# Performance work log

Measured on AMD Instinct MI355X. Metric: run time of the kernel, lower is better.

Reference implementation:

```python
import jax
import jax.numpy as jnp
from jax import lax
import numpy as np

EPS = 1e-5
CLASS_COUNT = 1000

# conv specs: (out_c, in_c, k, pool_stride)
_SPECS = [(8, 1, 11, 1), (32, 8, 7, 2), (64, 32, 5, 2), (64, 64, 5, 2), (128, 64, 5, 2), (128, 128, 3, 2)]


def _maxpool3(x, stride):
    return lax.reduce_window(x, -jnp.inf, lax.max, (1, 1, 3, 3), (1, 1, stride, stride), 'VALID')


def _block(x, w, gamma, beta, pool_stride):
    # tanh soft-binarized weights (mode=1, w=1)
    wq = jnp.tanh(w)
    y = lax.conv_general_dilated(x, wq, (1, 1), 'VALID', dimension_numbers=('NCHW', 'OIHW', 'NCHW'))
    y = _maxpool3(y, pool_stride)
    # BatchNorm2d in training mode: batch statistics over (N,H,W), biased var
    mu = jnp.mean(y, axis=(0, 2, 3), keepdims=True)
    var = jnp.var(y, axis=(0, 2, 3), keepdims=True)
    y = (y - mu) * lax.rsqrt(var + EPS)
    y = y * gamma.reshape(1, -1, 1, 1) + beta.reshape(1, -1, 1, 1)
    # tanh soft-binarized activation (mode=1, w=1)
    return jnp.tanh(y)


def setup_inputs() -> dict:
    key = jax.random.key(0)
    keys = jax.random.split(key, 8)
    inp = {'x': jax.random.normal(keys[0], (128, 1, 227, 227), dtype=jnp.float32)}
    for i, (oc, ic, k, _) in enumerate(_SPECS):
        fan_in = ic * k * k
        inp[f'w{i+1}'] = jax.random.normal(keys[i + 1], (oc, ic, k, k), dtype=jnp.float32) / np.sqrt(fan_in)
        inp[f'g{i+1}'] = jnp.ones((oc,), dtype=jnp.float32)
        inp[f'b{i+1}'] = jnp.zeros((oc,), dtype=jnp.float32)
    inp['wl'] = jax.random.normal(keys[7], (CLASS_COUNT, 512), dtype=jnp.float32) / np.sqrt(512.0)
    return inp


def reference(x, w1, w2, w3, w4, w5, w6, g1, g2, g3, g4, g5, g6,
              b1, b2, b3, b4, b5, b6, wl):
    ws = (w1, w2, w3, w4, w5, w6)
    gs = (g1, g2, g3, g4, g5, g6)
    bs = (b1, b2, b3, b4, b5, b6)
    for i, (_, _, _, ps) in enumerate(_SPECS):
        x = _block(x, ws[i], gs[i], bs[i], ps)
    # flatten -> BinaryLinear (tanh-binarized weight, no bias)
    x = x.reshape(x.shape[0], -1)  # [B, 512]
    return x @ jnp.tanh(wl).T  # [B, classCount]
```

## Files before the change

### kernel.cpp

```cpp
#include <hip/hip_runtime.h>
#include <hip/hip_bf16.h>
#include <hip/hip_fp16.h>

using bf16 = __hip_bfloat16;
using f16  = _Float16;
using f16x8 = __attribute__((ext_vector_type(8))) _Float16;
using f32x4  = __attribute__((ext_vector_type(4))) float;
typedef unsigned long long u64;

__device__ __forceinline__ float b2f(bf16 v){ return __bfloat162float(v); }
__device__ __forceinline__ bf16 f2b(float v){ return __float2bfloat16(v); }
__device__ __forceinline__ float ldf(const float* p){ return *p; }
__device__ __forceinline__ float ldf(const bf16* p){ return b2f(*p); }
__device__ __forceinline__ float ldf(const __half* p){ return __half2float(*p); }
__device__ __forceinline__ void stf(float* p, float v){ *p = v; }
__device__ __forceinline__ void stf(bf16* p, float v){ *p = f2b(v); }
__device__ __forceinline__ void stf(__half* p, float v){ *p = __float2half(v); }

__device__ __forceinline__ float ftanh(float x){
    float t = __builtin_amdgcn_exp2f(x * 2.8853900817779268f);
    return 1.0f - 2.0f * __builtin_amdgcn_rcpf(t + 1.0f);
}

__device__ __forceinline__ float ld_any(const void* p, int i, int isBf16)
{
    return isBf16 ? b2f(((const bf16*)p)[i]) : ((const float*)p)[i];
}

__device__ __forceinline__ int det_bf(const void* g)
{
    return (*(const unsigned*)g == 0x3F803F80u) ? 1 : 0;
}

__device__ __forceinline__ void bn_pr(const float* __restrict__ sums,
                                      const void* __restrict__ g,
                                      const void* __restrict__ b,
                                      int bf, int C, float inv, int c,
                                      float& sc, float& sh)
{
    float mean = sums[c] * inv;
    float var  = sums[C + c] * inv - mean * mean;
    float rstd = rsqrtf(fmaxf(var, 0.f) + 1e-5f);
    sc = ld_any(g, c, bf) * rstd;
    sh = ld_any(b, c, bf) - mean * sc;
}

__global__ __launch_bounds__(256)
void prep_all(const void* __restrict__ w1, const void* __restrict__ w6,
              const void* __restrict__ wlw, const void* __restrict__ w2,
              const void* __restrict__ w3, const void* __restrict__ w4,
              const void* __restrict__ w5, const void* __restrict__ g1,
              float* __restrict__ wq0, float* __restrict__ wq5,
              float* __restrict__ wlqT, __half* __restrict__ wpk,
              __half* __restrict__ wpk3, __half* __restrict__ wpk4,
              __half* __restrict__ wpk5, int* __restrict__ flag)
{
    const int bf = det_bf(g1);
    const int b = blockIdx.x, t = threadIdx.x;
    if (b == 0 && t == 0) *flag = bf;
    if (b < 4) {
        int i = b * 256 + t;
        if (i < 968) wq0[i] = tanhf(ld_any(w1, i, bf));
    } else if (b < 580) {
        int i = (b - 4) * 256 + t;
        if (i < 147456) wq5[i] = tanhf(ld_any(w6, i, bf));
    } else if (b < 2580) {
        int i = (b - 580) * 256 + t;
        if (i < 512000) {
            int cls = i >> 9, k = i & 511;
            wlqT[k * 1000 + cls] = tanhf(ld_any(wlw, i, bf));
        }
    } else if (b < 2636) {
        int i = (b - 2580) * 256 + t;
        if (i < 14336) {
            int ic  = i & 7;
            int q   = (i >> 3) & 3;
            int col = (i >> 5) & 15;
            int g   = (i >> 9) & 1;
            int khg = (i >> 10) & 1;
            int kw  = i >> 11;
            int kh  = khg * 4 + q;
            int oc  = g * 16 + col;
            __half v = __float2half(0.f);
            if (kh < 7)
                v = __float2half(tanhf(ld_any(w2, (oc * 8 + ic) * 49 + kh * 7 + kw, bf)));
            wpk[i] = v;
        }
    } else if (b < 2836) {
        int i = (b - 2636) * 256 + t;
        if (i < 51200) {
            int tap = i >> 11;
            int g   = (i >> 9) & 3;
            int col = (i >> 5) & 15;
            int icp = i & 31;
            int oc  = g * 16 + col;
            wpk3[i] = __float2half(tanhf(ld_any(w3, (oc * 32 + icp) * 25 + tap, bf)));
        }
    } else if (b < 3236) {
        int i = (b - 2836) * 256 + t;
        if (i < 102400) {
            int step = i >> 11;
            int g    = (i >> 9) & 3;
            int col  = (i >> 5) & 15;
            int icp  = i & 31;
            int icg  = step / 25, tap = step - icg * 25;
            int oc   = g * 16 + col;
            int ic   = icg * 32 + icp;
            wpk4[i] = __float2half(tanhf(ld_any(w4, (oc * 64 + ic) * 25 + tap, bf)));
        }
    } else {
        int i = (b - 3236) * 256 + t;
        if (i < 204800) {
            int step = i >> 12;
            int ocg  = (i >> 11) & 1;
            int g    = (i >> 9) & 3;
            int col  = (i >> 5) & 15;
            int icp  = i & 31;
            int icg  = step / 25, tap = step - icg * 25;
            int oc   = ocg * 64 + g * 16 + col;
            int ic   = icg * 32 + icp;
            wpk5[i] = __float2half(tanhf(ld_any(w5, (oc * 64 + ic) * 25 + tap, bf)));
        }
    }
}

__global__ __launch_bounds__(256)
void b2conv(const __half* __restrict__ A1, const __half* __restrict__ wpk,
            __half* __restrict__ raw, float* __restrict__ sums2,
            const float* __restrict__ sums1, const void* __restrict__ g1,
            const void* __restrict__ b1)
{
    __shared__ __align__(16) char smem[32000];
    __shared__ float s_part[512];
    f16*   xs = (f16*)smem;
    float* pb = (float*)smem;

    const int tid = threadIdx.x;
    const int n   = blockIdx.z;
    const int ty  = blockIdx.x / 15, tx = blockIdx.x - ty * 15;
    const int cy0 = ty * 30, cx0 = tx * 14;

    const int bf1 = det_bf(g1);
    float ssc[8], ssh[8];
    #pragma unroll
    for (int j = 0; j < 8; j++)
        bn_pr(sums1, g1, b1, bf1, 8, 1.f / 5916800.f, j, ssc[j], ssh[j]);

    for (int i = tid; i < 858; i += 256) {
        int r = i / 22, c = i - r * 22;
        int gr = cy0 + r, gc = cx0 + c;
        f16x8 v = (f16x8){0, 0, 0, 0, 0, 0, 0, 0};
        if (gr < 215 && gc < 215)
            v = *(const f16x8*)((const f16*)A1 + ((size_t)(n * 215 + gr) * 215 + gc) * 8);
        f16x8 o;
        #pragma unroll
        for (int j = 0; j < 8; j++)
            o[j] = (f16)ftanh(fmaf((float)v[j], ssc[j], ssh[j]));
        *(f16x8*)(xs + i * 8) = o;
    }
    __syncthreads();

    const int lane = tid & 63, wid = tid >> 6;
    const int col = lane & 15, q = lane >> 4;
    const int arow = q * 22;

    f32x4 acc[8][2];
    #pragma unroll
    for (int f = 0; f < 8; f++)
        #pragma unroll
        for (int g = 0; g < 2; g++)
            acc[f][g] = (f32x4){0.f, 0.f, 0.f, 0.f};

    const f16* wb = (const f16*)wpk + col * 32 + q * 8;
    f16x8 wc0 = *(const f16x8*)(wb);
    f16x8 wc1 = *(const f16x8*)(wb + 512);

    #pragma unroll
    for (int s = 0; s < 14; s++) {
        f16x8 wn0 = wc0, wn1 = wc1;
        if (s < 13) {
            const f16* wn = wb + (s + 1) * 1024;
            wn0 = *(const f16x8*)(wn);
            wn1 = *(const f16x8*)(wn + 512);
        }
        int kw = s >> 1, khg = s & 1;
        int aoffs = arow + khg * 88 + kw;
        #pragma unroll
        for (int f = 0; f < 8; f++) {
            int gi = (wid * 8 + f) * 22 + col + aoffs;
            f16x8 a = *(const f16x8*)(xs + gi * 8);
            acc[f][0] = __builtin_amdgcn_mfma_f32_16x16x32_f16(a, wc0, acc[f][0], 0, 0, 0);
            acc[f][1] = __builtin_amdgcn_mfma_f32_16x16x32_f16(a, wc1, acc[f][1], 0, 0, 0);
        }
        wc0 = wn0; wc1 = wn1;
    }
    __syncthreads();

    for (int h = 0; h < 2; h++) {
        #pragma unroll
        for (int f = 0; f < 8; f++) {
            int cr = wid * 8 + f;
            if (cr < 31)
                *(f32x4*)(pb + col * 500 + cr * 16 + q * 4) = acc[f][h];
        }
        __syncthreads();
        const int ocl = tid >> 4, slot = tid & 15;
        float sm = 0.f, sq = 0.f;
        for (int j = slot; j < 105; j += 16) {
            int py = j / 7, px = j - (j / 7) * 7;
            int gph = ty * 15 + py, gpw = tx * 7 + px;
            if (gph < 104 && gpw < 104) {
                const float* cp = pb + ocl * 500 + (2 * py) * 16 + 2 * px;
                float m = cp[0];
                #pragma unroll
                for (int dy = 0; dy < 3; dy++)
                    #pragma unroll
                    for (int dx = 0; dx < 3; dx++)
                        m = fmaxf(m, cp[dy * 16 + dx]);
                int oc = h * 16 + ocl;
                size_t oidx = ((size_t)(n * 104 + gph) * 104 + gpw) * 32 + oc;
                raw[oidx] = __float2half(m);
                sm += m; sq += m * m;
            }
        }
        s_part[tid] = sm; s_part[256 + tid] = sq;
        __syncthreads();
        if (tid < 16) {
            float a = 0.f, b = 0.f;
            #pragma unroll
            for (int t = 0; t < 16; t++) {
                a += s_part[tid * 16 + t];
                b += s_part[256 + tid * 16 + t];
            }
            atomicAdd(&sums2[h * 16 + tid],      a);
            atomicAdd(&sums2[32 + h * 16 + tid], b);
        }
        __syncthreads();
    }
}

__global__ __launch_bounds__(256)
void b3conv(const __half* __restrict__ A2, const __half* __restrict__ wpk3,
            __half* __restrict__ A3t, float* __restrict__ sums3,
            const float* __restrict__ sums2, const void* __restrict__ g2,
            const void* __restrict__ b2)
{
    __shared__ __align__(16) char smem[32000];
    __shared__ float s_part[512];
    f16*   xs = (f16*)smem;
    float* pb = (float*)smem;

    const int tid = threadIdx.x;
    const int n   = blockIdx.z;
    const int ty  = blockIdx.x / 7, tx = blockIdx.x - ty * 7;
    const int y0  = ty * 14, x0 = tx * 14;

    if (tid < 32) {
        float sc, sh;
        bn_pr(sums2, g2, b2, det_bf(g2), 32, 1.f / 1384448.f, tid, sc, sh);
        s_part[tid] = sc; s_part[32 + tid] = sh;
    }
    __syncthreads();

    for (int i = tid; i < 1600; i += 256) {
        int pos = i >> 2, g8 = i & 3;
        int gy = y0 + pos / 20, gx = x0 + pos % 20;
        f16x8 v = *(const f16x8*)((const f16*)A2 +
                  ((size_t)(n * 104 + gy) * 104 + gx) * 32 + g8 * 8);
        int c0 = g8 * 8;
        f16x8 o;
        #pragma unroll
        for (int j = 0; j < 8; j++)
            o[j] = (f16)ftanh(fmaf((float)v[j], s_part[c0 + j], s_part[32 + c0 + j]));
        *(f16x8*)(xs + pos * 40 + g8 * 8) = o;
    }

    const int lane = tid & 63, wid = tid >> 6;
    const int col = lane & 15, q = lane >> 4;

    f32x4 acc[4][4];
    #pragma unroll
    for (int f = 0; f < 4; f++)
        #pragma unroll
        for (int g = 0; g < 4; g++)
            acc[f][g] = (f32x4){0.f, 0.f, 0.f, 0.f};

    const f16* wb = (const f16*)wpk3 + col * 32 + q * 8;
    f16x8 w[4];
    #pragma unroll
    for (int g = 0; g < 4; g++)
        w[g] = *(const f16x8*)(wb + g * 512);

    __syncthreads();

    #pragma unroll 1
    for (int tap = 0; tap < 25; tap++) {
        const f16* wnb = wb + (tap < 24 ? tap + 1 : tap) * 2048;
        f16x8 wn[4];
        #pragma unroll
        for (int g = 0; g < 4; g++)
            wn[g] = *(const f16x8*)(wnb + g * 512);

        int kh = tap / 5, kw = tap - (tap / 5) * 5;
        f16x8 a[4];
        #pragma unroll
        for (int f = 0; f < 4; f++) {
            int pos = (wid * 4 + f + kh) * 20 + col + kw;
            a[f] = *(const f16x8*)(xs + pos * 40 + q * 8);
        }
        #pragma unroll
        for (int g = 0; g < 4; g++)
            #pragma unroll
            for (int f = 0; f < 4; f++)
                acc[f][g] = __builtin_amdgcn_mfma_f32_16x16x32_f16(
                    a[f], w[g], acc[f][g], 0, 0, 0);
        #pragma unroll
        for (int g = 0; g < 4; g++)
            w[g] = wn[g];
    }

    for (int h = 0; h < 2; h++) {
        __syncthreads();
        #pragma unroll
        for (int f = 0; f < 4; f++) {
            int cr = wid * 4 + f;
            if (cr < 15) {
                #pragma unroll
                for (int gg = 0; gg < 2; gg++)
                    *(f32x4*)(pb + (gg * 16 + col) * 244 + cr * 16 + q * 4) = acc[f][h * 2 + gg];
            }
        }
        __syncthreads();
        const int ocl = tid >> 3, slot = tid & 7;
        float sm = 0.f, sq = 0.f;
        for (int j = slot; j < 49; j += 8) {
            int py = j / 7, px = j - (j / 7) * 7;
            const float* cp = pb + ocl * 244 + (2 * py) * 16 + 2 * px;
            float m = cp[0];
            #pragma unroll
            for (int dy = 0; dy < 3; dy++)
                #pragma unroll
                for (int dx = 0; dx < 3; dx++)
                    m = fmaxf(m, cp[dy * 16 + dx]);
            int gph = ty * 7 + py, gpw = tx * 7 + px;
            A3t[((size_t)(n * 49 + gph) * 49 + gpw) * 64 + h * 32 + ocl]
                = __float2half(m);
            sm += m; sq += m * m;
        }
        s_part[tid] = sm; s_part[256 + tid] = sq;
        __syncthreads();
        if (tid < 32) {
            float a = 0.f, b = 0.f;
            #pragma unroll
            for (int t = 0; t < 8; t++) {
                a += s_part[tid * 8 + t];
                b += s_part[256 + tid * 8 + t];
            }
            atomicAdd(&sums3[h * 32 + tid],      a);
            atomicAdd(&sums3[64 + h * 32 + tid], b);
        }
    }
}

__global__ __launch_bounds__(256)
void b4conv(const __half* __restrict__ A3t, const __half* __restrict__ wpk4,
            __half* __restrict__ A4, float* __restrict__ sums4,
            const float* __restrict__ sums3, const void* __restrict__ g3,
            const void* __restrict__ b3)
{
    __shared__ __align__(16) char smem[31232];
    __shared__ float s_part[512];
    __shared__ float s_ss[128];
    f16*   xs = (f16*)smem;
    float* pb = (float*)smem;

    const int tid = threadIdx.x;
    const int n   = blockIdx.z;
    const int ty  = blockIdx.x >> 2, tx = blockIdx.x & 3;
    const int y0  = ty * 14, x0 = tx * 14;
    const int lane = tid & 63, wid = tid >> 6;
    const int col = lane & 15, q = lane >> 4;

    if (tid < 64) {
        float sc, sh;
        bn_pr(sums3, g3, b3, det_bf(g3), 64, 1.f / 307328.f, tid, sc, sh);
        s_ss[tid] = sc; s_ss[64 + tid] = sh;
    }

    f32x4 acc[4][4];
    #pragma unroll
    for (int f = 0; f < 4; f++)
        #pragma unroll
        for (int g = 0; g < 4; g++)
            acc[f][g] = (f32x4){0.f, 0.f, 0.f, 0.f};

    const f16* wb = (const f16*)wpk4 + col * 32 + q * 8;
    f16x8 w[4];
    #pragma unroll
    for (int g = 0; g < 4; g++)
        w[g] = *(const f16x8*)(wb + g * 512);

    #pragma unroll 1
    for (int icg = 0; icg < 2; icg++) {
        __syncthreads();
        for (int i = tid; i < 1520; i += 256) {
            int pos = i >> 2, g8 = i & 3;
            int gy = y0 + pos / 20, gx = x0 + pos % 20;
            f16x8 o = (f16x8){0, 0, 0, 0, 0, 0, 0, 0};
            if (gy < 49 && gx < 49) {
                f16x8 v = *(const f16x8*)((const f16*)A3t +
                    ((size_t)(n * 49 + gy) * 49 + gx) * 64 + icg * 32 + g8 * 8);
                int c0 = icg * 32 + g8 * 8;
                #pragma unroll
                for (int j = 0; j < 8; j++)
                    o[j] = (f16)ftanh(fmaf((float)v[j], s_ss[c0 + j], s_ss[64 + c0 + j]));
            }
            *(f16x8*)(xs + pos * 40 + g8 * 8) = o;
        }
        __syncthreads();

        #pragma unroll 1
        for (int tap = 0; tap < 25; tap++) {
            int step = icg * 25 + tap;
            const f16* wnb = wb + (size_t)(step < 49 ? step + 1 : step) * 2048;
            f16x8 wn[4];
            #pragma unroll
            for (int g = 0; g < 4; g++)
                wn[g] = *(const f16x8*)(wnb + g * 512);

            int kh = tap / 5, kw = tap - (tap / 5) * 5;
            f16x8 a[4];
            #pragma unroll
            for (int f = 0; f < 4; f++) {
                int r = wid * 4 + f + kh; if (r > 18) r = 18;
                int pos = r * 20 + col + kw;
                a[f] = *(const f16x8*)(xs + pos * 40 + q * 8);
            }
            #pragma unroll
            for (int g = 0; g < 4; g++)
                #pragma unroll
                for (int f = 0; f < 4; f++)
                    acc[f][g] = __builtin_amdgcn_mfma_f32_16x16x32_f16(
                        a[f], w[g], acc[f][g], 0, 0, 0);
            #pragma unroll
            for (int g = 0; g < 4; g++)
                w[g] = wn[g];
        }
    }

    for (int h = 0; h < 2; h++) {
        __syncthreads();
        #pragma unroll
        for (int f = 0; f < 4; f++) {
            int cr = wid * 4 + f;
            if (cr < 15) {
                #pragma unroll
                for (int gg = 0; gg < 2; gg++)
                    *(f32x4*)(pb + (gg * 16 + col) * 244 + cr * 16 + q * 4) = acc[f][h * 2 + gg];
            }
        }
        __syncthreads();
        const int ocl = tid >> 3, slot = tid & 7;
        float sm = 0.f, sq = 0.f;
        for (int j = slot; j < 49; j += 8) {
            int py = j / 7, px = j - (j / 7) * 7;
            int gph = ty * 7 + py, gpw = tx * 7 + px;
            if (gph < 22 && gpw < 22) {
                const float* cp = pb + ocl * 244 + (2 * py) * 16 + 2 * px;
                float m = cp[0];
                #pragma unroll
                for (int dy = 0; dy < 3; dy++)
                    #pragma unroll
                    for (int dx = 0; dx < 3; dx++)
                        m = fmaxf(m, cp[dy * 16 + dx]);
                A4[((size_t)(n * 22 + gph) * 22 + gpw) * 64 + h * 32 + ocl]
                    = __float2half(m);
                sm += m; sq += m * m;
            }
        }
        s_part[tid] = sm; s_part[256 + tid] = sq;
        __syncthreads();
        if (tid < 32) {
            float a = 0.f, b = 0.f;
            #pragma unroll
            for (int t = 0; t < 8; t++) {
                a += s_part[tid * 8 + t];
                b += s_part[256 + tid * 8 + t];
            }
            atomicAdd(&sums4[h * 32 + tid],      a);
            atomicAdd(&sums4[64 + h * 32 + tid], b);
        }
    }
}

__global__ __launch_bounds__(256)
void b5conv(const __half* __restrict__ A4, const __half* __restrict__ wpk5,
            float* __restrict__ A5, float* __restrict__ sums5,
            const float* __restrict__ sums4, const void* __restrict__ g4,
            const void* __restrict__ b4)
{
    __shared__ __align__(16) char smem[49664];
    __shared__ float s_part[512];
    __shared__ float s_ss[128];
    f16*   xs = (f16*)smem;
    float* pb = (float*)smem;

    const int tid = threadIdx.x;
    const int n   = blockIdx.z;
    const int ocg = blockIdx.x;
    const int lane = tid & 63, wid = tid >> 6;
    const int col = lane & 15, q = lane >> 4;

    if (tid < 64) {
        float sc, sh;
        bn_pr(sums4, g4, b4, det_bf(g4), 64, 1.f / 61952.f, tid, sc, sh);
        s_ss[tid] = sc; s_ss[64 + tid] = sh;
    }

    int abase[6];
    #pragma unroll
    for (int f = 0; f < 6; f++) {
        int m = (wid * 6 + f) * 16 + col;
        if (m > 323) m = 323;
        int r = m / 18, cc = m - r * 18;
        abase[f] = r * 22 + cc;
    }

    f32x4 acc[6][4];
    #pragma unroll
    for (int f = 0; f < 6; f++)
        #pragma unroll
        for (int g = 0; g < 4; g++)
            acc[f][g] = (f32x4){0.f, 0.f, 0.f, 0.f};

    const f16* wb = (const f16*)wpk5 + ocg * 2048 + col * 32 + q * 8;
    f16x8 w[4];
    #pragma unroll
    for (int g = 0; g < 4; g++)
        w[g] = *(const f16x8*)(wb + g * 512);

    #pragma unroll 1
    for (int icg = 0; icg < 2; icg++) {
        __syncthreads();
        for (int i = tid; i < 1936; i += 256) {
            int pos = i >> 2, g8 = i & 3;
            f16x8 v = *(const f16x8*)((const f16*)A4 + ((size_t)(n * 484 + pos)) * 64
                                      + icg * 32 + g8 * 8);
            int c0 = icg * 32 + g8 * 8;
            f16x8 o;
            #pragma unroll
            for (int j = 0; j < 8; j++)
                o[j] = (f16)ftanh(fmaf((float)v[j], s_ss[c0 + j], s_ss[64 + c0 + j]));
            *(f16x8*)(xs + pos * 40 + g8 * 8) = o;
        }
        __syncthreads();

        #pragma unroll 1
        for (int tap = 0; tap < 25; tap++) {
            int step = icg * 25 + tap;
            const f16* wnb = wb + (size_t)(step < 49 ? step + 1 : step) * 4096;
            f16x8 wn[4];
            #pragma unroll
            for (int g = 0; g < 4; g++)
                wn[g] = *(const f16x8*)(wnb + g * 512);

            int kh = tap / 5, kw = tap - (tap / 5) * 5;
            int off = kh * 22 + kw;
            f16x8 a[6];
            #pragma unroll
            for (int f = 0; f < 6; f++)
                a[f] = *(const f16x8*)(xs + (abase[f] + off) * 40 + q * 8);
            #pragma unroll
            for (int g = 0; g < 4; g++)
                #pragma unroll
                for (int f = 0; f < 6; f++)
                    acc[f][g] = __builtin_amdgcn_mfma_f32_16x16x32_f16(
                        a[f], w[g], acc[f][g], 0, 0, 0);
            #pragma unroll
            for (int g = 0; g < 4; g++)
                w[g] = wn[g];
        }
    }

    for (int h = 0; h < 2; h++) {
        __syncthreads();
        #pragma unroll
        for (int f = 0; f < 6; f++)
            #pragma unroll
            for (int gg = 0; gg < 2; gg++)
                *(f32x4*)(pb + (gg * 16 + col) * 388 + (wid * 6 + f) * 16 + q * 4)
                    = acc[f][h * 2 + gg];
        __syncthreads();
        const int ocl = tid >> 3, slot = tid & 7;
        float sm = 0.f, sq = 0.f;
        for (int j = slot; j < 64; j += 8) {
            int py = j >> 3, px = j & 7;
            const float* cp = pb + ocl * 388 + (2 * py) * 18 + 2 * px;
            float m = cp[0];
            #pragma unroll
            for (int dy = 0; dy < 3; dy++)
                #pragma unroll
                for (int dx = 0; dx < 3; dx++)
                    m = fmaxf(m, cp[dy * 18 + dx]);
            int oc = ocg * 64 + h * 32 + ocl;
            A5[((size_t)(n * 128 + oc) * 8 + py) * 8 + px] = m;
            sm += m; sq += m * m;
        }
        s_part[tid] = sm; s_part[256 + tid] = sq;
        __syncthreads();
        if (tid < 32) {
            float a = 0.f, b = 0.f;
            #pragma unroll
            for (int t = 0; t < 8; t++) {
                a += s_part[tid * 8 + t];
                b += s_part[256 + tid * 8 + t];
            }
            int oc = ocg * 64 + h * 32 + tid;
            atomicAdd(&sums5[oc],       a);
            atomicAdd(&sums5[128 + oc], b);
        }
    }
}

__global__ __launch_bounds__(256)
void bn_tanh_flat(float* __restrict__ x, const float* __restrict__ sums,
                  const void* __restrict__ g, const void* __restrict__ b, int n)
{
    int idx = blockIdx.x * 256 + threadIdx.x;
    if (idx >= n) return;
    int c = (idx >> 6) & 127;
    float sc, sh;
    bn_pr(sums, g, b, det_bf(g), 128, 1.f / 8192.f, c, sc, sh);
    x[idx] = ftanh(fmaf(x[idx], sc, sh));
}

template<int K>
__global__ __launch_bounds__(256)
void convpool_s(const float* __restrict__ in, const float* __restrict__ wq,
                float* __restrict__ out, float* __restrict__ sums,
                int IC, int OC, int PS, int Hin, int Win, int PH, int PW, int total)
{
    int idx = blockIdx.x * 256 + threadIdx.x;
    if (idx >= total) return;
    int pw = idx % PW;
    int t1 = idx / PW;
    int ph = t1 % PH;
    int t2 = t1 / PH;
    int oc = t2 % OC;
    int n  = t2 / OC;
    const int by = ph * PS, bx = pw * PS;

    float acc[3][3];
    #pragma unroll
    for (int a = 0; a < 3; a++)
        #pragma unroll
        for (int b = 0; b < 3; b++) acc[a][b] = 0.f;

    const float* wp = wq + oc * IC * K * K;
    const float* np = in + (n * IC) * Hin * Win;

    #pragma unroll 1
    for (int ic = 0; ic < IC; ic++) {
        const float* xp = np + ic * Hin * Win;
        const float* wc = wp + ic * K * K;
        #pragma unroll
        for (int r = 0; r < K + 2; r++) {
            float xr[K + 2];
            const float* xrow = xp + (by + r) * Win + bx;
            #pragma unroll
            for (int j = 0; j < K + 2; j++) xr[j] = xrow[j];
            #pragma unroll
            for (int dy = 0; dy < 3; dy++) {
                const int kh = r - dy;
                if (0 <= kh && kh < K) {
                    const float* wrow = wc + kh * K;
                    #pragma unroll
                    for (int kw = 0; kw < K; kw++) {
                        float w = wrow[kw];
                        acc[dy][0] = fmaf(w, xr[kw + 0], acc[dy][0]);
                        acc[dy][1] = fmaf(w, xr[kw + 1], acc[dy][1]);
                        acc[dy][2] = fmaf(w, xr[kw + 2], acc[dy][2]);
                    }
                }
            }
        }
    }
    float m = acc[0][0];
    #pragma unroll
    for (int a = 0; a < 3; a++)
        #pragma unroll
        for (int b = 0; b < 3; b++) m = fmaxf(m, acc[a][b]);
    out[idx] = m;

    float s1 = m, s2 = m * m;
    s1 += __shfl_xor(s1, 1); s2 += __shfl_xor(s2, 1);
    s1 += __shfl_xor(s1, 2); s2 += __shfl_xor(s2, 2);
    if ((threadIdx.x & 3) == 0) {
        atomicAdd(&sums[oc],      s1);
        atomicAdd(&sums[OC + oc], s2);
    }
}

template<int MODE, int RAWIN, int IC, int OC, int K, int PS, int TPH, int TPW,
         int OCB, int OCT, int CIC, int NP, bool ONHWC, typename InT, typename OutT>
__global__ __launch_bounds__(256)
void ctile(const void* __restrict__ in, const float* __restrict__ wq,
           OutT* __restrict__ out, float* __restrict__ sums,
           const float* __restrict__ ss, const void* __restrict__ g1in,
           int Hin, int Win, int PH, int PW, int tilesX)
{
    constexpr int TPO  = OCB / OCT;
    constexpr int CH   = PS * (TPH - 1) + 3;
    constexpr int CW   = PS * (TPW - 1) + 3;
    constexpr int SPR  = (CW + NP - 1) / NP;
    constexpr int CWP  = SPR * NP;
    constexpr int NSTR = CH * SPR;
    static_assert(NSTR * TPO <= 256, "thread mapping overflow");
    constexpr int IH   = CH + K - 1;
    constexpr int IW   = CW + K - 1;
    constexpr int IWE_ = (CWP + K - 1 > IW) ? (CWP + K - 1) : IW;
    constexpr int IWE  = IWE_ | 1;
    constexpr int IN_SZ  = CIC * IH * IWE;
    constexpr int INP    = (IN_SZ + 3) & ~3;
    constexpr int W_SZ   = CIC * K * K * OCB;
    constexpr int CONV_SZ = OCB * CH * CWP;
    constexpr int LDS_SZ = (INP + W_SZ > CONV_SZ) ? (INP + W_SZ) : CONV_SZ;

    __shared__ __align__(16) float lds[LDS_SZ];
    __shared__ float s_part[512];

    const int tid = threadIdx.x;
    const int n   = blockIdx.z;
    const int oc0 = blockIdx.y * OCB;
    const int tY  = blockIdx.x / tilesX;
    const int tX  = blockIdx.x - tY * tilesX;
    const int ph0 = tY * TPH, pw0 = tX * TPW;
    const int ih0 = ph0 * PS, iw0 = pw0 * PS;

    const int bfin = RAWIN ? det_bf(g1in) : 0;

    const int  og  = tid % TPO;
    const int  s   = tid / TPO;
    const bool act = (s < NSTR);
    const int  r   = s / SPR;
    const int  c0  = (s - r * SPR) * NP;

    float acc[NP][OCT];
    #pragma unroll
    for (int p = 0; p < NP; p++)
        #pragma unroll
        for (int o = 0; o < OCT; o++) acc[p][o] = 0.f;

    for (int icb = 0; icb < IC; icb += CIC) {
        for (int idx = tid; idx < IN_SZ; idx += 256) {
            int ic  = idx / (IH * IWE);
            int rem = idx - ic * (IH * IWE);
            int rr  = rem / IWE, cc = rem - rr * IWE;
            int gr  = ih0 + rr, gc = iw0 + cc;
            float v = 0.f;
            if (gr < Hin && gc < Win) {
                size_t gidx = ((size_t)(n * IC + icb + ic) * Hin + gr) * Win + gc;
                v = RAWIN ? ld_any(in, (int)gidx, bfin) : ldf(&((const InT*)in)[gidx]);
            }
            lds[idx] = v;
        }
        for (int idx = tid; idx < W_SZ; idx += 256) {
            int ocl = idx % OCB;
            int kk  = (idx / OCB) % (K * K);
            int c_  = idx / (OCB * K * K);
            lds[INP + idx] = wq[((size_t)(oc0 + ocl) * IC + icb + c_) * (K * K) + kk];
        }
        __syncthreads();

        if (act) {
            #pragma unroll 1
            for (int ic_ = 0; ic_ < CIC; ic_++) {
                const float* xb = lds + ic_ * (IH * IWE);
                const float* wb = lds + INP + ic_ * (K * K * OCB) + og * OCT;
                #pragma unroll 1
                for (int kh = 0; kh < K; kh++) {
                    const float* xr = xb + (r + kh) * IWE + c0;
                    float xwin[NP + K - 1];
                    #pragma unroll
                    for (int j = 0; j < NP + K - 1; j++) xwin[j] = xr[j];
                    #pragma unroll
                    for (int kw = 0; kw < K; kw++) {
                        const float* wp2 = wb + (kh * K + kw) * OCB;
                        float wv[OCT];
                        #pragma unroll
                        for (int o = 0; o < OCT; o += 4) {
                            float4 t = *(const float4*)(wp2 + o);
                            wv[o] = t.x; wv[o+1] = t.y; wv[o+2] = t.z; wv[o+3] = t.w;
                        }
                        #pragma unroll
                        for (int p = 0; p < NP; p++)
                            #pragma unroll
                            for (int o = 0; o < OCT; o++)
                                acc[p][o] = fmaf(wv[o], xwin[p + kw], acc[p][o]);
                    }
                }
            }
        }
        __syncthreads();
    }

    if (act) {
        #pragma unroll
        for (int p = 0; p < NP; p++)
            #pragma unroll
            for (int o = 0; o < OCT; o++)
                lds[(og * OCT + o) * (CH * CWP) + r * CWP + c0 + p] = acc[p][o];
    }
    __syncthreads();

    {
        constexpr int TPC = 256 / OCB;
        const int ocl = tid / TPC, slot = tid - ocl * TPC;
        float sm = 0.f, sq = 0.f;
        for (int j = slot; j < TPH * TPW; j += TPC) {
            int py = j / TPW, px = j - (j / TPW) * TPW;
            int gph = ph0 + py, gpw = pw0 + px;
            if (gph < PH && gpw < PW) {
                const float* cp = lds + ocl * (CH * CWP) + (py * PS) * CWP + px * PS;
                float m = cp[0];
                #pragma unroll
                for (int dy = 0; dy < 3; dy++)
                    #pragma unroll
                    for (int dx = 0; dx < 3; dx++)
                        m = fmaxf(m, cp[dy * CWP + dx]);
                size_t oidx = ONHWC
                    ? ((size_t)(n * PH + gph) * PW + gpw) * OC + oc0 + ocl
                    : ((size_t)(n * OC + oc0 + ocl) * PH + gph) * PW + gpw;
                if (MODE == 2) {
                    int c = oc0 + ocl;
                    stf(&out[oidx], ftanh(fmaf(m, ss[c], ss[OC + c])));
                } else {
                    if (MODE == 0) stf(&out[oidx], m);
                    sm += m; sq += m * m;
                }
            }
        }
        if (MODE != 2) {
            s_part[tid] = sm; s_part[256 + tid] = sq;
            __syncthreads();
            if (tid < OCB) {
                float a = 0.f, b = 0.f;
                #pragma unroll
                for (int t = 0; t < TPC; t++) {
                    a += s_part[tid * TPC + t];
                    b += s_part[256 + tid * TPC + t];
                }
                atomicAdd(&sums[oc0 + tid],      a);
                atomicAdd(&sums[OC + oc0 + tid], b);
            }
        }
    }
}

__global__ __launch_bounds__(256)
void linear_k(const float* __restrict__ act, const float* __restrict__ wlqT,
              void* __restrict__ out, const int* __restrict__ flag,
              const float* __restrict__ sums6, const void* __restrict__ g6,
              const void* __restrict__ b6)
{
    __shared__ float s_a[512];
    __shared__ float s_ss[256];
    int bf = *flag;
    int tid = threadIdx.x;
    if (tid < 128) {
        float sc, sh;
        bn_pr(sums6, g6, b6, bf, 128, 1.f / 512.f, tid, sc, sh);
        s_ss[tid] = sc; s_ss[128 + tid] = sh;
    }
    __syncthreads();
    int n = blockIdx.y;
    for (int i = tid; i < 512; i += 256) {
        int c = i >> 2;
        s_a[i] = ftanh(fmaf(act[n * 512 + i], s_ss[c], s_ss[128 + c]));
    }
    __syncthreads();
    int cls = blockIdx.x * 256 + tid;
    if (cls < 1000) {
        float acc = 0.f;
        #pragma unroll 8
        for (int k = 0; k < 512; k++)
            acc = fmaf(s_a[k], wlqT[k * 1000 + cls], acc);
        if (bf) ((bf16*)out)[n * 1000 + cls] = f2b(acc);
        else    ((float*)out)[n * 1000 + cls] = acc;
    }
}

extern "C" void kernel_launch(void* const* d_in, const int* in_sizes, int n_in,
                              void* d_out, int out_size, void* d_ws, size_t ws_size,
                              hipStream_t stream)
{
    (void)in_sizes; (void)n_in; (void)out_size; (void)ws_size;
    const void* x = d_in[0];
    const void* W[6]; const void* G[6]; const void* B[6];
    for (int i = 0; i < 6; i++) {
        W[i] = d_in[1 + 3 * i];
        G[i] = d_in[2 + 3 * i];
        B[i] = d_in[3 + 3 * i];
    }
    const void* wl = d_in[19];

    char* p = (char*)d_ws;
    auto carve = [&](size_t bytes) -> void* {
        void* r = (void*)p;
        p += (bytes + 255) & ~((size_t)255);
        return r;
    };
    int*   flag = (int*)carve(256);
    const int wsz[6] = {968, 12544, 51200, 102400, 204800, 147456};
    float* wq[6];
    for (int i = 0; i < 6; i++) wq[i] = (float*)carve((size_t)wsz[i] * 4);
    float* wlqT = (float*)carve((size_t)512000 * 4);
    float* sums_all = (float*)carve(1536 * 4);
    float* S1 = sums_all;        float* S2 = sums_all + 256;
    float* S3 = sums_all + 512;  float* S4 = sums_all + 768;
    float* S5 = sums_all + 1024; float* S6 = sums_all + 1280;
    __half* wpk  = (__half*)carve((size_t)14336 * 2);
    __half* wpk3 = (__half*)carve((size_t)51200 * 2);
    __half* wpk4 = (__half*)carve((size_t)102400 * 2);
    __half* wpk5 = (__half*)carve((size_t)204800 * 2);
    __half* R1  = (__half*)carve((size_t)47334400 * 2);
    __half* R2  = (__half*)carve((size_t)44302336 * 2);
    __half* A1  = R1;
    __half* A2  = R2;
    __half* A3t = R1;
    __half* A4  = R2;
    float*  A5  = (float*)R1;
    float*  A6  = (float*)R2;

    auto cdiv = [](int a, int b) { return (a + b - 1) / b; };

    hipMemsetAsync(sums_all, 0, 1536 * 4, stream);
    prep_all<<<4036, 256, 0, stream>>>(W[0], W[5], wl, W[1], W[2], W[3], W[4], G[0],
                                       wq[0], wq[5], wlqT, wpk, wpk3, wpk4, wpk5, flag);

    ctile<0, 1, 1, 8, 11, 1, 34, 40, 8, 8, 1, 7, true, float, __half>
        <<<dim3(42, 1, 128), 256, 0, stream>>>(x, wq[0], A1, S1, S1, G[0], 227, 227, 215, 215, 6);

    b2conv<<<dim3(105, 1, 128), 256, 0, stream>>>(A1, wpk, A2, S2, S1, G[0], B[0]);

    b3conv<<<dim3(49, 1, 128), 256, 0, stream>>>(A2, wpk3, A3t, S3, S2, G[1], B[1]);

    b4conv<<<dim3(16, 1, 128), 256, 0, stream>>>(A3t, wpk4, A4, S4, S3, G[2], B[2]);

    b5conv<<<dim3(2, 1, 128), 256, 0, stream>>>(A4, wpk5, A5, S5, S4, G[3], B[3]);
    bn_tanh_flat<<<cdiv(1048576, 256), 256, 0, stream>>>(A5, S5, G[4], B[4], 1048576);

    convpool_s<3><<<cdiv(65536, 256), 256, 0, stream>>>(
        A5, wq[5], A6, S6, 128, 128, 2, 8, 8, 2, 2, 65536);

    linear_k<<<dim3(4, 128), 256, 0, stream>>>(A6, wlqT, d_out, flag, S6, G[5], B[5]);
}
```

Baseline: 1.274 ms.

## Replace scalar layer-1 conv with fp16 MFMA kernel using packed weights

The first convolution (1->8 channels, 11x11, stride-1 maxpool) now runs in a dedicated MFMA kernel instead of the generic scalar-FMA tiled kernel. The prep kernel packs the tanh-quantized 11x11 weights into zero-padded 16x32 fp16 MFMA operand tiles. The input is staged in LDS as fp16 with eight shifted copies, so each lane reads aligned 8-wide vectors. The maxpool and batch-stat partial sums are then done through LDS. This cuts layer-1 FMA instruction count, but rounds input and weights to fp16 and wastes half the MFMA N dimension, since only 8 of 16 columns are real channels.

Result: slower. 1.376 ms (+8.0%).

```diff
diff --git a/kernel.cpp b/kernel.cpp
--- a/kernel.cpp
+++ b/kernel.cpp
@@ -53,7 +53,8 @@
               float* __restrict__ wq0, float* __restrict__ wq5,
               float* __restrict__ wlqT, __half* __restrict__ wpk,
               __half* __restrict__ wpk3, __half* __restrict__ wpk4,
-              __half* __restrict__ wpk5, int* __restrict__ flag)
+              __half* __restrict__ wpk5, __half* __restrict__ wpk1m,
+              int* __restrict__ flag)
 {
     const int bf = det_bf(g1);
     const int b = blockIdx.x, t = threadIdx.x;
@@ -108,7 +109,7 @@
             int ic   = icg * 32 + icp;
             wpk4[i] = __float2half(tanhf(ld_any(w4, (oc * 64 + ic) * 25 + tap, bf)));
         }
-    } else {
+    } else if (b < 4036) {
         int i = (b - 3236) * 256 + t;
         if (i < 204800) {
             int step = i >> 12;
@@ -121,6 +122,123 @@
             int ic   = icg * 32 + icp;
             wpk5[i] = __float2half(tanhf(ld_any(w5, (oc * 64 + ic) * 25 + tap, bf)));
         }
+    } else {
+        int i = (b - 4036) * 256 + t;
+        if (i < 3072) {
+            int e  = i & 7;
+            int nn = (i >> 3) & 15;
+            int q  = (i >> 7) & 3;
+            int st = i >> 9;
+            int kh = 2 * st + (q >> 1);
+            int kw = (q & 1) * 8 + e;
+            __half v = __float2half(0.f);
+            if (nn < 8 && kh < 11 && kw < 11)
+                v = __float2half(tanhf(ld_any(w1, nn * 121 + kh * 11 + kw, bf)));
+            wpk1m[i] = v;
+        }
+    }
+}
+
+__global__ __launch_bounds__(256)
+void b1conv_m(const void* __restrict__ x, const __half* __restrict__ wpk1m,
+              __half* __restrict__ A1, float* __restrict__ sums1,
+              const void* __restrict__ g1in)
+{
+    __shared__ __align__(16) char smem[38016];
+    __shared__ float s_part[512];
+    f16*   xs = (f16*)smem;
+    float* pb = (float*)smem;
+
+    const int tid  = threadIdx.x;
+    const int n    = blockIdx.z;
+    const int trow = blockIdx.x >> 2, tcol = blockIdx.x & 3;
+    const int pr0  = trow * 14, pc0 = tcol * 56;
+    const int bfin = det_bf(g1in);
+
+    for (int it = tid; it < 2160; it += 256) {
+        int s   = it / 270;
+        int rem = it - s * 270;
+        int row = rem / 10;
+        int ib  = (rem - row * 10) * 8;
+        int gr  = pr0 + row;
+        f16 v[8];
+        #pragma unroll
+        for (int e = 0; e < 8; e++) {
+            int gc = pc0 + ib + e + s;
+            float f = 0.f;
+            if (gr < 227 && gc < 227)
+                f = ld_any(x, (n * 227 + gr) * 227 + gc, bfin);
+            v[e] = (f16)f;
+        }
+        *(f16x8*)(xs + (s * 27 + row) * 88 + ib) = *(f16x8*)v;
+    }
+
+    const int lane = tid & 63, w = tid >> 6;
+    const int col = lane & 15, q = lane >> 4;
+    const int wc0 = w * 14;
+    const int khh = q >> 1, kwb = q & 1;
+
+    f16x8 bw[6];
+    #pragma unroll
+    for (int st = 0; st < 6; st++)
+        bw[st] = *(const f16x8*)((const f16*)wpk1m + ((st * 4 + q) * 16 + col) * 8);
+
+    __syncthreads();
+
+    f32x4 accv[16];
+    #pragma unroll 1
+    for (int c = 0; c < 16; c++) {
+        int cxs   = wc0 + c;
+        int s     = cxs & 7;
+        int ibase = (cxs & ~7) + 8 * kwb;
+        const f16* base = xs + s * 27 * 88 + ibase;
+        f32x4 acc = (f32x4){0.f, 0.f, 0.f, 0.f};
+        #pragma unroll
+        for (int st = 0; st < 6; st++) {
+            int row = col + 2 * st + khh;
+            f16x8 a = *(const f16x8*)(base + row * 88);
+            acc = __builtin_amdgcn_mfma_f32_16x16x32_f16(a, bw[st], acc, 0, 0, 0);
+        }
+        accv[c] = acc;
+    }
+
+    __syncthreads();
+
+    if (col < 8) {
+        #pragma unroll
+        for (int c = 0; c < 14; c++) {
+            #pragma unroll
+            for (int j = 0; j < 4; j++) {
+                float hm = fmaxf(fmaxf(accv[c][j], accv[c + 1][j]), accv[c + 2][j]);
+                pb[(col * 16 + q * 4 + j) * 59 + wc0 + c] = hm;
+            }
+        }
+    }
+    __syncthreads();
+
+    const int oc = tid >> 5, slot = tid & 31;
+    float sm = 0.f, sq = 0.f;
+    for (int jj = slot; jj < 784; jj += 32) {
+        int pr = jj / 56, pcc = jj - pr * 56;
+        int gr = pr0 + pr, gc = pc0 + pcc;
+        if (gr < 215 && gc < 215) {
+            const float* cp = pb + (oc * 16 + pr) * 59 + pcc;
+            float m = fmaxf(fmaxf(cp[0], cp[59]), cp[118]);
+            A1[((size_t)(n * 215 + gr) * 215 + gc) * 8 + oc] = __float2half(m);
+            sm += m; sq += m * m;
+        }
+    }
+    s_part[tid] = sm; s_part[256 + tid] = sq;
+    __syncthreads();
+    if (tid < 8) {
+        float a = 0.f, b = 0.f;
+        #pragma unroll
+        for (int t = 0; t < 32; t++) {
+            a += s_part[tid * 32 + t];
+            b += s_part[256 + tid * 32 + t];
+        }
+        atomicAdd(&sums1[tid],     a);
+        atomicAdd(&sums1[8 + tid], b);
     }
 }
 
@@ -701,162 +819,6 @@
     }
 }
 
-template<int MODE, int RAWIN, int IC, int OC, int K, int PS, int TPH, int TPW,
-         int OCB, int OCT, int CIC, int NP, bool ONHWC, typename InT, typename OutT>
-__global__ __launch_bounds__(256)
-void ctile(const void* __restrict__ in, const float* __restrict__ wq,
-           OutT* __restrict__ out, float* __restrict__ sums,
-           const float* __restrict__ ss, const void* __restrict__ g1in,
-           int Hin, int Win, int PH, int PW, int tilesX)
-{
-    constexpr int TPO  = OCB / OCT;
-    constexpr int CH   = PS * (TPH - 1) + 3;
-    constexpr int CW   = PS * (TPW - 1) + 3;
-    constexpr int SPR  = (CW + NP - 1) / NP;
-    constexpr int CWP  = SPR * NP;
-    constexpr int NSTR = CH * SPR;
-    static_assert(NSTR * TPO <= 256, "thread mapping overflow");
-    constexpr int IH   = CH + K - 1;
-    constexpr int IW   = CW + K - 1;
-    constexpr int IWE_ = (CWP + K - 1 > IW) ? (CWP + K - 1) : IW;
-    constexpr int IWE  = IWE_ | 1;
-    constexpr int IN_SZ  = CIC * IH * IWE;
-    constexpr int INP    = (IN_SZ + 3) & ~3;
-    constexpr int W_SZ   = CIC * K * K * OCB;
-    constexpr int CONV_SZ = OCB * CH * CWP;
-    constexpr int LDS_SZ = (INP + W_SZ > CONV_SZ) ? (INP + W_SZ) : CONV_SZ;
-
-    __shared__ __align__(16) float lds[LDS_SZ];
-    __shared__ float s_part[512];
-
-    const int tid = threadIdx.x;
-    const int n   = blockIdx.z;
-    const int oc0 = blockIdx.y * OCB;
-    const int tY  = blockIdx.x / tilesX;
-    const int tX  = blockIdx.x - tY * tilesX;
-    const int ph0 = tY * TPH, pw0 = tX * TPW;
-    const int ih0 = ph0 * PS, iw0 = pw0 * PS;
-
-    const int bfin = RAWIN ? det_bf(g1in) : 0;
-
-    const int  og  = tid % TPO;
-    const int  s   = tid / TPO;
-    const bool act = (s < NSTR);
-    const int  r   = s / SPR;
-    const int  c0  = (s - r * SPR) * NP;
-
-    float acc[NP][OCT];
-    #pragma unroll
-    for (int p = 0; p < NP; p++)
-        #pragma unroll
-        for (int o = 0; o < OCT; o++) acc[p][o] = 0.f;
-
-    for (int icb = 0; icb < IC; icb += CIC) {
-        for (int idx = tid; idx < IN_SZ; idx += 256) {
-            int ic  = idx / (IH * IWE);
-            int rem = idx - ic * (IH * IWE);
-            int rr  = rem / IWE, cc = rem - rr * IWE;
-            int gr  = ih0 + rr, gc = iw0 + cc;
-            float v = 0.f;
-            if (gr < Hin && gc < Win) {
-                size_t gidx = ((size_t)(n * IC + icb + ic) * Hin + gr) * Win + gc;
-                v = RAWIN ? ld_any(in, (int)gidx, bfin) : ldf(&((const InT*)in)[gidx]);
-            }
-            lds[idx] = v;
-        }
-        for (int idx = tid; idx < W_SZ; idx += 256) {
-            int ocl = idx % OCB;
-            int kk  = (idx / OCB) % (K * K);
-            int c_  = idx / (OCB * K * K);
-            lds[INP + idx] = wq[((size_t)(oc0 + ocl) * IC + icb + c_) * (K * K) + kk];
-        }
-        __syncthreads();
-
-        if (act) {
-            #pragma unroll 1
-            for (int ic_ = 0; ic_ < CIC; ic_++) {
-                const float* xb = lds + ic_ * (IH * IWE);
-                const float* wb = lds + INP + ic_ * (K * K * OCB) + og * OCT;
-                #pragma unroll 1
-                for (int kh = 0; kh < K; kh++) {
-                    const float* xr = xb + (r + kh) * IWE + c0;
-                    float xwin[NP + K - 1];
-                    #pragma unroll
-                    for (int j = 0; j < NP + K - 1; j++) xwin[j] = xr[j];
-                    #pragma unroll
-                    for (int kw = 0; kw < K; kw++) {
-                        const float* wp2 = wb + (kh * K + kw) * OCB;
-                        float wv[OCT];
-                        #pragma unroll
-                        for (int o = 0; o < OCT; o += 4) {
-                            float4 t = *(const float4*)(wp2 + o);
-                            wv[o] = t.x; wv[o+1] = t.y; wv[o+2] = t.z; wv[o+3] = t.w;
-                        }
-                        #pragma unroll
-                        for (int p = 0; p < NP; p++)
-                            #pragma unroll
-                            for (int o = 0; o < OCT; o++)
-                                acc[p][o] = fmaf(wv[o], xwin[p + kw], acc[p][o]);
-                    }
-                }
-            }
-        }
-        __syncthreads();
-    }
-
-    if (act) {
-        #pragma unroll
-        for (int p = 0; p < NP; p++)
-            #pragma unroll
-            for (int o = 0; o < OCT; o++)
-                lds[(og * OCT + o) * (CH * CWP) + r * CWP + c0 + p] = acc[p][o];
-    }
-    __syncthreads();
-
-    {
-        constexpr int TPC = 256 / OCB;
-        const int ocl = tid / TPC, slot = tid - ocl * TPC;
-        float sm = 0.f, sq = 0.f;
-        for (int j = slot; j < TPH * TPW; j += TPC) {
-            int py = j / TPW, px = j - (j / TPW) * TPW;
-            int gph = ph0 + py, gpw = pw0 + px;
-            if (gph < PH && gpw < PW) {
-                const float* cp = lds + ocl * (CH * CWP) + (py * PS) * CWP + px * PS;
-                float m = cp[0];
-                #pragma unroll
-                for (int dy = 0; dy < 3; dy++)
-                    #pragma unroll
-                    for (int dx = 0; dx < 3; dx++)
-                        m = fmaxf(m, cp[dy * CWP + dx]);
-                size_t oidx = ONHWC
-                    ? ((size_t)(n * PH + gph) * PW + gpw) * OC + oc0 + ocl
-                    : ((size_t)(n * OC + oc0 + ocl) * PH + gph) * PW + gpw;
-                if (MODE == 2) {
-                    int c = oc0 + ocl;
-                    stf(&out[oidx], ftanh(fmaf(m, ss[c], ss[OC + c])));
-                } else {
-                    if (MODE == 0) stf(&out[oidx], m);
-                    sm += m; sq += m * m;
-                }
-            }
-        }
-        if (MODE != 2) {
-            s_part[tid] = sm; s_part[256 + tid] = sq;
-            __syncthreads();
-            if (tid < OCB) {
-                float a = 0.f, b = 0.f;
-                #pragma unroll
-                for (int t = 0; t < TPC; t++) {
-                    a += s_part[tid * TPC + t];
-                    b += s_part[256 + tid * TPC + t];
-                }
-                atomicAdd(&sums[oc0 + tid],      a);
-                atomicAdd(&sums[OC + oc0 + tid], b);
-            }
-        }
-    }
-}
-
 __global__ __launch_bounds__(256)
 void linear_k(const float* __restrict__ act, const float* __restrict__ wlqT,
               void* __restrict__ out, const int* __restrict__ flag,
@@ -919,10 +881,11 @@
     float* S1 = sums_all;        float* S2 = sums_all + 256;
     float* S3 = sums_all + 512;  float* S4 = sums_all + 768;
     float* S5 = sums_all + 1024; float* S6 = sums_all + 1280;
-    __half* wpk  = (__half*)carve((size_t)14336 * 2);
-    __half* wpk3 = (__half*)carve((size_t)51200 * 2);
-    __half* wpk4 = (__half*)carve((size_t)102400 * 2);
-    __half* wpk5 = (__half*)carve((size_t)204800 * 2);
+    __half* wpk   = (__half*)carve((size_t)14336 * 2);
+    __half* wpk3  = (__half*)carve((size_t)51200 * 2);
+    __half* wpk4  = (__half*)carve((size_t)102400 * 2);
+    __half* wpk5  = (__half*)carve((size_t)204800 * 2);
+    __half* wpk1m = (__half*)carve((size_t)3072 * 2);
     __half* R1  = (__half*)carve((size_t)47334400 * 2);
     __half* R2  = (__half*)carve((size_t)44302336 * 2);
     __half* A1  = R1;
@@ -935,11 +898,11 @@
     auto cdiv = [](int a, int b) { return (a + b - 1) / b; };
 
     hipMemsetAsync(sums_all, 0, 1536 * 4, stream);
-    prep_all<<<4036, 256, 0, stream>>>(W[0], W[5], wl, W[1], W[2], W[3], W[4], G[0],
-                                       wq[0], wq[5], wlqT, wpk, wpk3, wpk4, wpk5, flag);
-
-    ctile<0, 1, 1, 8, 11, 1, 34, 40, 8, 8, 1, 7, true, float, __half>
-        <<<dim3(42, 1, 128), 256, 0, stream>>>(x, wq[0], A1, S1, S1, G[0], 227, 227, 215, 215, 6);
+    prep_all<<<4048, 256, 0, stream>>>(W[0], W[5], wl, W[1], W[2], W[3], W[4], G[0],
+                                       wq[0], wq[5], wlqT, wpk, wpk3, wpk4, wpk5,
+                                       wpk1m, flag);
+
+    b1conv_m<<<dim3(64, 1, 128), 256, 0, stream>>>(x, wpk1m, A1, S1, G[0]);
 
     b2conv<<<dim3(105, 1, 128), 256, 0, stream>>>(A1, wpk, A2, S2, S1, G[0], B[0]);
 
```
